# Kernel optimization log

Measured on AMD Instinct MI355X. Metric: run time of the kernel, lower is better.

## Reference

```python
import jax, jax.numpy as jnp
import numpy as np

MAX_EMBED = 1024
MAX_HEADS = 16
MIN_WIDTH_RATIO = 0.25


def setup_inputs() -> dict:
    key = jax.random.key(0)
    ks = jax.random.split(key, 10)
    B, S, E = 4, 1024, MAX_EMBED
    query = jax.random.normal(ks[0], (B, S, E), dtype=jnp.float32)
    attention_mask = jax.random.randint(ks[1], (B, 1, 1, S), 0, 2, dtype=jnp.int32)
    # SlimmableLinear params (max sizes); kaiming-ish scale ~ 1/sqrt(fan_in)
    scale = 1.0 / np.sqrt(E)
    def lin(kw, kb):
        w = jax.random.uniform(kw, (E, E), dtype=jnp.float32, minval=-scale, maxval=scale)
        b = jax.random.uniform(kb, (E,), dtype=jnp.float32, minval=-scale, maxval=scale)
        return w, b
    q_w, q_b = lin(ks[2], ks[3])
    k_w, k_b = lin(ks[4], ks[5])
    v_w, v_b = lin(ks[6], ks[7])
    o_w, o_b = lin(ks[8], ks[9])
    return {"query": query, "attention_mask": attention_mask,
            "q_w": q_w, "q_b": q_b, "k_w": k_w, "k_b": k_b,
            "v_w": v_w, "v_b": v_b, "o_w": o_w, "o_b": o_b,
            "width": 768}


def _slim_linear(x, w, b, width):
    # weight stored [out, in] like torch; slice to [width, width]
    return x[..., :width] @ w[:width, :width].T + b[:width]


def reference(query, attention_mask, q_w, q_b, k_w, k_b, v_w, v_b, o_w, o_b, width):
    min_width = int(MAX_EMBED * MIN_WIDTH_RATIO)
    width = max(min_width, min(int(width), MAX_EMBED))
    num_heads = max(1, width * MAX_HEADS // MAX_EMBED)
    head_dim = width // num_heads
    B, S, _ = query.shape

    q = _slim_linear(query, q_w, q_b, width)  # [B,S,width]
    k = _slim_linear(query, k_w, k_b, width)  # key=query (self-attn)
    v = _slim_linear(query, v_w, v_b, width)

    q = q.reshape(B, S, num_heads, head_dim).transpose(0, 2, 1, 3)  # [B,H,S,D]
    k = k.reshape(B, S, num_heads, head_dim).transpose(0, 2, 1, 3)
    v = v.reshape(B, S, num_heads, head_dim).transpose(0, 2, 1, 3)

    scores = jnp.einsum('bhqd,bhkd->bhqk', q, k) / jnp.sqrt(jnp.float32(head_dim))
    scores = jnp.where(attention_mask == 0, jnp.float32(-1e9), scores)
    attn_weights = jax.nn.softmax(scores, axis=-1)  # [B,H,S,S]
    attn_output = jnp.einsum('bhqk,bhkd->bhqd', attn_weights, v)
    attn_output = attn_output.transpose(0, 2, 1, 3).reshape(B, S, width)
    output = attn_output @ o_w[:width, :width].T + o_b[:width]
    return output, attn_weights
```

## Files before the change

kernel.cpp:

```cpp
#include <hip/hip_runtime.h>

#define Bn 4
#define Sn 1024
#define En 1024
#define Wn 768
#define Hn 12
#define Dn 64
#define XE ((size_t)Bn * Sn * Wn)

typedef __attribute__((ext_vector_type(8))) short short8;
typedef __attribute__((ext_vector_type(4))) short short4v;
typedef __attribute__((ext_vector_type(4))) float floatx4;

#define MFMA16(A, B, C) __builtin_amdgcn_mfma_f32_16x16x32_bf16(A, B, C, 0, 0, 0)

__device__ __forceinline__ unsigned short f2bf_rn(float f) {
    unsigned int u = __float_as_uint(f);
    unsigned int r = u + 0x7fffu + ((u >> 16) & 1u);
    return (unsigned short)(r >> 16);
}
__device__ __forceinline__ float bf2f(unsigned short h) {
    return __uint_as_float(((unsigned int)h) << 16);
}

__device__ __forceinline__ void gload_lds16(const unsigned short* g, unsigned short* l) {
    __builtin_amdgcn_global_load_lds(
        (const __attribute__((address_space(1))) void*)g,
        (__attribute__((address_space(3))) void*)l, 16, 0, 0);
}

__global__ __launch_bounds__(256) void prep_kernel(
    const float* __restrict__ x,
    const float* __restrict__ qw, const float* __restrict__ kw,
    const float* __restrict__ vw, const float* __restrict__ ow,
    const float* __restrict__ qb, const float* __restrict__ kb,
    const float* __restrict__ vb,
    unsigned short* __restrict__ xh, unsigned short* __restrict__ xl,
    unsigned short* __restrict__ wqh, unsigned short* __restrict__ wql,
    unsigned short* __restrict__ woh, unsigned short* __restrict__ wol,
    float* __restrict__ bq)
{
    const int bx = blockIdx.x;
    const float* src; unsigned short *dh, *dl; int e;
    if (bx < 3072) {
        e = (bx * 256 + threadIdx.x) * 4;
        src = x; dh = xh; dl = xl;
    } else if (bx < 3072 + 1728) {
        int bb = bx - 3072; int which = bb / 576;
        e = ((bb - which * 576) * 256 + threadIdx.x) * 4;
        src = (which == 0) ? qw : (which == 1) ? kw : vw;
        dh = wqh + (size_t)which * Wn * Wn;
        dl = wql + (size_t)which * Wn * Wn;
    } else if (bx < 3072 + 1728 + 576) {
        e = ((bx - 3072 - 1728) * 256 + threadIdx.x) * 4;
        src = ow; dh = woh; dl = wol;
    } else {
        int t = (bx - 3072 - 1728 - 576) * 256 + threadIdx.x;
        if (t < Wn) bq[t] = qb[t];
        else if (t < 2 * Wn) bq[t] = kb[t - Wn];
        else if (t < 3 * Wn) bq[t] = vb[t - 2 * Wn];
        return;
    }
    int row = e / Wn, col = e - row * Wn;
    float4 v = *(const float4*)(src + (size_t)row * En + col);
    float f[4] = {v.x, v.y, v.z, v.w};
    short4v h, l;
    #pragma unroll
    for (int i = 0; i < 4; ++i) {
        unsigned short hh = f2bf_rn(f[i]);
        h[i] = (short)hh;
        l[i] = (short)f2bf_rn(f[i] - bf2f(hh));
    }
    *(short4v*)(dh + e) = h;
    *(short4v*)(dl + e) = l;
}

__global__ __launch_bounds__(256) void qkv_mfma_kernel(
    const unsigned short* __restrict__ xh, const unsigned short* __restrict__ xl,
    const unsigned short* __restrict__ wh, const unsigned short* __restrict__ wl,
    const float* __restrict__ bq,
    unsigned short* __restrict__ qh_o, unsigned short* __restrict__ kh_o,
    unsigned short* __restrict__ vt_o)
{
    __shared__ __align__(16) unsigned short Ah[128 * 32];
    __shared__ __align__(16) unsigned short Al[128 * 32];
    __shared__ __align__(16) unsigned short Bh[128 * 32];
    __shared__ __align__(16) unsigned short Bl[128 * 32];

    const int tid = threadIdx.x;
    const int wave = tid >> 6, lane = tid & 63;
    const int quad = lane >> 4, l16 = lane & 15;
    const int m0 = blockIdx.x * 128, n0 = blockIdx.y * 128;
    const int wm = wave >> 1, wn = wave & 1;
    const int which = n0 / Wn;
    const bool full = (which == 2);

    floatx4 acc[4][4] = {};

    const unsigned short* gsrc = (wave == 0) ? xh : (wave == 1) ? xl
                               : (wave == 2) ? wh : wl;
    unsigned short* ldst = (wave == 0) ? Ah : (wave == 1) ? Al
                         : (wave == 2) ? Bh : Bl;
    const int base_row = (wave < 2) ? m0 : n0;
    const int r_in = lane >> 2;
    const int cs = (lane & 3) ^ (r_in & 3);

    for (int k0 = 0; k0 < Wn; k0 += 32) {
        if (full || wave != 1) {
            #pragma unroll
            for (int i = 0; i < 8; ++i) {
                int r = i * 16 + r_in;
                const unsigned short* gp =
                    gsrc + (size_t)(base_row + r) * Wn + k0 + cs * 8;
                gload_lds16(gp, ldst + i * 512);
            }
        }
        __syncthreads();

        short8 afh[4], afl[4], bfh[4], bfl[4];
        #pragma unroll
        for (int t = 0; t < 4; ++t) {
            int mr = wm * 64 + t * 16 + l16;
            int ca = quad ^ (mr & 3);
            afh[t] = *(const short8*)(Ah + mr * 32 + ca * 8);
            if (full) afl[t] = *(const short8*)(Al + mr * 32 + ca * 8);
            int nr = wn * 64 + t * 16 + l16;
            int cb = quad ^ (nr & 3);
            bfh[t] = *(const short8*)(Bh + nr * 32 + cb * 8);
            bfl[t] = *(const short8*)(Bl + nr * 32 + cb * 8);
        }
        #pragma unroll
        for (int mt = 0; mt < 4; ++mt)
            #pragma unroll
            for (int nt = 0; nt < 4; ++nt) {
                acc[mt][nt] = MFMA16(afh[mt], bfh[nt], acc[mt][nt]);
                acc[mt][nt] = MFMA16(afh[mt], bfl[nt], acc[mt][nt]);
                if (full) acc[mt][nt] = MFMA16(afl[mt], bfh[nt], acc[mt][nt]);
            }
        __syncthreads();
    }

    const int b = m0 >> 10;
    #pragma unroll
    for (int nt = 0; nt < 4; ++nt) {
        const int ng = n0 + wn * 64 + nt * 16 + l16;
        const float bias = bq[ng];
        const int f = ng - which * Wn;
        const int h = f >> 6, d = f & 63;
        #pragma unroll
        for (int mt = 0; mt < 4; ++mt) {
            const int mbase = m0 + wm * 64 + mt * 16 + quad * 4;
            const int s0 = mbase & (Sn - 1);
            if (which < 2) {
                unsigned short* oq = which ? kh_o : qh_o;
                size_t idx = (((size_t)(b * Hn + h)) * Sn + s0) * Dn + d;
                #pragma unroll
                for (int r = 0; r < 4; ++r)
                    oq[idx + (size_t)r * Dn] = f2bf_rn(acc[mt][nt][r] + bias);
            } else {
                size_t idx = (((size_t)(b * Hn + h)) * Dn + d) * Sn + s0;
                short4v pk;
                #pragma unroll
                for (int r = 0; r < 4; ++r)
                    pk[r] = (short)f2bf_rn(acc[mt][nt][r] + bias);
                *(short4v*)(vt_o + idx) = pk;
            }
        }
    }
}

__global__ __launch_bounds__(256) void attn_sum_kernel(
    const unsigned short* __restrict__ qh, const unsigned short* __restrict__ kh,
    const int* __restrict__ mask, float* __restrict__ lpart)
{
    const int tid = threadIdx.x;
    const int wave = tid >> 6, lane = tid & 63;
    const int quad = lane >> 4, l16 = lane & 15;
    const int qt = blockIdx.x >> 2, ks = blockIdx.x & 3;
    const int h = blockIdx.y, b = blockIdx.z;
    const int bh = b * Hn + h;
    const size_t kvb = (size_t)bh * Sn * Dn;

    short8 qf[2];
    {
        const int s = qt * 64 + wave * 16 + l16;
        const unsigned short* qp = qh + kvb + (size_t)s * Dn + quad * 8;
        qf[0] = *(const short8*)(qp);
        qf[1] = *(const short8*)(qp + 32);
    }

    float lsum[4] = {0.f, 0.f, 0.f, 0.f};

    for (int kt = 0; kt < 4; ++kt) {
        #pragma unroll
        for (int ct = 0; ct < 4; ++ct) {
            const int key = ks * 256 + kt * 64 + ct * 16 + l16;
            const unsigned short* kp = kh + kvb + (size_t)key * Dn + quad * 8;
            short8 kf0 = *(const short8*)(kp);
            short8 kf1 = *(const short8*)(kp + 32);
            floatx4 acc = {0.f, 0.f, 0.f, 0.f};
            acc = MFMA16(qf[0], kf0, acc);
            acc = MFMA16(qf[1], kf1, acc);
            const float mv = (float)mask[b * Sn + key];
            #pragma unroll
            for (int r = 0; r < 4; ++r)
                lsum[r] += __expf(acc[r] * 0.125f) * mv;
        }
    }

    #pragma unroll
    for (int r = 0; r < 4; ++r) {
        float v = lsum[r];
        v += __shfl_xor(v, 1, 64);
        v += __shfl_xor(v, 2, 64);
        v += __shfl_xor(v, 4, 64);
        v += __shfl_xor(v, 8, 64);
        lsum[r] = v;
    }
    if (l16 == 0) {
        const int row = qt * 64 + wave * 16 + quad * 4;
        #pragma unroll
        for (int r = 0; r < 4; ++r)
            lpart[((size_t)ks * Bn * Hn + bh) * Sn + row + r] = lsum[r];
    }
}

__global__ __launch_bounds__(256) void attn_out_kernel(
    const unsigned short* __restrict__ qh, const unsigned short* __restrict__ kh,
    const unsigned short* __restrict__ vt, const int* __restrict__ mask,
    const float* __restrict__ lpart, float* __restrict__ attn,
    unsigned short* __restrict__ aoh, unsigned short* __restrict__ aol)
{
    __shared__ __align__(16) unsigned short Ps[4][16 * 72];

    const int tid = threadIdx.x;
    const int wave = tid >> 6, lane = tid & 63;
    const int quad = lane >> 4, l16 = lane & 15;
    const int qt = blockIdx.x;
    const int h = blockIdx.y, b = blockIdx.z;
    const int bh = b * Hn + h;
    const size_t kvb = (size_t)bh * Sn * Dn;
    const size_t vbase = (size_t)bh * Dn * Sn;

    short8 qf[2];
    {
        const int s = qt * 64 + wave * 16 + l16;
        const unsigned short* qp = qh + kvb + (size_t)s * Dn + quad * 8;
        qf[0] = *(const short8*)(qp);
        qf[1] = *(const short8*)(qp + 32);
    }

    const int row0 = qt * 64 + wave * 16 + quad * 4;
    float li[4];
    #pragma unroll
    for (int r = 0; r < 4; ++r) {
        float lv = 0.f;
        #pragma unroll
        for (int s4 = 0; s4 < 4; ++s4)
            lv += lpart[((size_t)s4 * Bn * Hn + bh) * Sn + row0 + r];
        li[r] = (lv > 0.f) ? 1.f / lv : 0.f;
    }

    floatx4 oacc[4] = {};

    for (int kk = 0; kk < 16; ++kk) {
        const int k0 = kk * 64;
        #pragma unroll
        for (int ct = 0; ct < 4; ++ct) {
            const int key = k0 + ct * 16 + l16;
            const unsigned short* kp = kh + kvb + (size_t)key * Dn + quad * 8;
            short8 kf0 = *(const short8*)(kp);
            short8 kf1 = *(const short8*)(kp + 32);
            floatx4 acc = {0.f, 0.f, 0.f, 0.f};
            acc = MFMA16(qf[0], kf0, acc);
            acc = MFMA16(qf[1], kf1, acc);
            const float mv = (float)mask[b * Sn + key];
            #pragma unroll
            for (int r = 0; r < 4; ++r) {
                const float p = __expf(acc[r] * 0.125f) * mv * li[r];
                attn[((size_t)bh * Sn + row0 + r) * Sn + key] = p;
                Ps[wave][(quad * 4 + r) * 72 + ct * 16 + l16] = f2bf_rn(p);
            }
        }
        #pragma unroll
        for (int ksp = 0; ksp < 2; ++ksp) {
            short8 pf = *(const short8*)&Ps[wave][l16 * 72 + ksp * 32 + quad * 8];
            #pragma unroll
            for (int dt = 0; dt < 4; ++dt) {
                short8 vf = *(const short8*)(vt + vbase
                              + (size_t)(dt * 16 + l16) * Sn + k0 + ksp * 32 + quad * 8);
                oacc[dt] = MFMA16(pf, vf, oacc[dt]);
            }
        }
    }

    #pragma unroll
    for (int dt = 0; dt < 4; ++dt) {
        #pragma unroll
        for (int r = 0; r < 4; ++r) {
            const float o = oacc[dt][r];
            const unsigned short hh = f2bf_rn(o);
            const size_t idx = ((size_t)b * Sn + row0 + r) * Wn + h * Dn + dt * 16 + l16;
            aoh[idx] = hh;
            aol[idx] = f2bf_rn(o - bf2f(hh));
        }
    }
}

__global__ __launch_bounds__(256) void oproj_mfma_kernel(
    const unsigned short* __restrict__ aoh, const unsigned short* __restrict__ aol,
    const unsigned short* __restrict__ wh, const unsigned short* __restrict__ wl,
    const float* __restrict__ ob, float* __restrict__ out)
{
    __shared__ __align__(16) unsigned short Ah[64 * 32];
    __shared__ __align__(16) unsigned short Al[64 * 32];
    __shared__ __align__(16) unsigned short Bh[128 * 32];
    __shared__ __align__(16) unsigned short Bl[128 * 32];

    const int tid = threadIdx.x;
    const int wave = tid >> 6, lane = tid & 63;
    const int quad = lane >> 4, l16 = lane & 15;
    const int m0 = blockIdx.x * 64, n0 = blockIdx.y * 128;
    const int wm = wave >> 1, wn = wave & 1;

    floatx4 acc[2][4] = {};

    const int r_in = lane >> 2;
    const int cs = (lane & 3) ^ (r_in & 3);

    for (int k0 = 0; k0 < Wn; k0 += 32) {
        if (wave == 0) {
            #pragma unroll
            for (int i = 0; i < 4; ++i) {
                gload_lds16(aoh + (size_t)(m0 + i * 16 + r_in) * Wn + k0 + cs * 8,
                            Ah + i * 512);
                gload_lds16(aol + (size_t)(m0 + i * 16 + r_in) * Wn + k0 + cs * 8,
                            Al + i * 512);
            }
        } else if (wave == 1) {
            #pragma unroll
            for (int i = 0; i < 8; ++i)
                gload_lds16(wh + (size_t)(n0 + i * 16 + r_in) * Wn + k0 + cs * 8,
                            Bh + i * 512);
        } else if (wave == 2) {
            #pragma unroll
            for (int i = 0; i < 8; ++i)
                gload_lds16(wl + (size_t)(n0 + i * 16 + r_in) * Wn + k0 + cs * 8,
                            Bl + i * 512);
        }
        __syncthreads();

        short8 afh[2], afl[2], bfh[4], bfl[4];
        #pragma unroll
        for (int t = 0; t < 2; ++t) {
            int mr = wm * 32 + t * 16 + l16;
            int ca = quad ^ (mr & 3);
            afh[t] = *(const short8*)(Ah + mr * 32 + ca * 8);
            afl[t] = *(const short8*)(Al + mr * 32 + ca * 8);
        }
        #pragma unroll
        for (int t = 0; t < 4; ++t) {
            int nr = wn * 64 + t * 16 + l16;
            int cb = quad ^ (nr & 3);
            bfh[t] = *(const short8*)(Bh + nr * 32 + cb * 8);
            bfl[t] = *(const short8*)(Bl + nr * 32 + cb * 8);
        }
        #pragma unroll
        for (int mt = 0; mt < 2; ++mt)
            #pragma unroll
            for (int nt = 0; nt < 4; ++nt) {
                acc[mt][nt] = MFMA16(afh[mt], bfh[nt], acc[mt][nt]);
                acc[mt][nt] = MFMA16(afh[mt], bfl[nt], acc[mt][nt]);
                acc[mt][nt] = MFMA16(afl[mt], bfh[nt], acc[mt][nt]);
            }
        __syncthreads();
    }

    #pragma unroll
    for (int nt = 0; nt < 4; ++nt) {
        const int ng = n0 + wn * 64 + nt * 16 + l16;
        const float bias = ob[ng];
        #pragma unroll
        for (int mt = 0; mt < 2; ++mt) {
            const int m = m0 + wm * 32 + mt * 16 + quad * 4;
            #pragma unroll
            for (int r = 0; r < 4; ++r)
                out[(size_t)(m + r) * Wn + ng] = acc[mt][nt][r] + bias;
        }
    }
}

extern "C" void kernel_launch(void* const* d_in, const int* in_sizes, int n_in,
                              void* d_out, int out_size, void* d_ws, size_t ws_size,
                              hipStream_t stream) {
    const float* x    = (const float*)d_in[0];
    const int*   mask = (const int*)  d_in[1];
    const float* qw = (const float*)d_in[2];
    const float* qb = (const float*)d_in[3];
    const float* kw = (const float*)d_in[4];
    const float* kb = (const float*)d_in[5];
    const float* vw = (const float*)d_in[6];
    const float* vb = (const float*)d_in[7];
    const float* ow = (const float*)d_in[8];
    const float* ob = (const float*)d_in[9];

    float* out  = (float*)d_out;
    float* attn = out + XE;

    char* w = (char*)d_ws;
    unsigned short* xh   = (unsigned short*)w;  w += XE * 2;
    unsigned short* xl   = (unsigned short*)w;  w += XE * 2;
    unsigned short* wqh  = (unsigned short*)w;  w += (size_t)3 * Wn * Wn * 2;
    unsigned short* wql  = (unsigned short*)w;  w += (size_t)3 * Wn * Wn * 2;
    unsigned short* woh  = (unsigned short*)w;  w += (size_t)Wn * Wn * 2;
    unsigned short* wol  = (unsigned short*)w;  w += (size_t)Wn * Wn * 2;
    float*          bq   = (float*)w;           w += (size_t)3 * Wn * 4;
    unsigned short* qh   = (unsigned short*)w;  w += XE * 2;
    unsigned short* kh   = (unsigned short*)w;  w += XE * 2;
    unsigned short* vt_w = (unsigned short*)w;  w += XE * 2;
    float*          lpart = (float*)w;          w += (size_t)4 * Bn * Hn * Sn * 4;

    prep_kernel<<<5385, 256, 0, stream>>>(x, qw, kw, vw, ow, qb, kb, vb,
                                          xh, xl, wqh, wql, woh, wol, bq);

    qkv_mfma_kernel<<<dim3(32, 18), 256, 0, stream>>>(
        xh, xl, wqh, wql, bq, qh, kh, vt_w);

    attn_sum_kernel<<<dim3(64, Hn, Bn), 256, 0, stream>>>(
        qh, kh, mask, lpart);

    attn_out_kernel<<<dim3(16, Hn, Bn), 256, 0, stream>>>(
        qh, kh, vt_w, mask, lpart, attn, xh, xl);

    oproj_mfma_kernel<<<dim3(64, 6), 256, 0, stream>>>(
        xh, xl, woh, wol, ob, out);
}
```

Baseline: 462.5 us.

## Drop low-part MFMAs for Q/K, stage mask in LDS, vectorize attn writes from bf16

The QKV projection now runs only the hi*hi MFMA for the Q and K outputs and skips loading the low-part weight tiles, keeping the three-term split only for V. Both attention kernels stage the mask into shared memory as floats instead of re-reading the int mask per key. The attention-weights output is now written as row-contiguous float4 stores taken from the bf16-rounded P tile in LDS, replacing scattered per-element fp32 stores. These changes cut MFMA work, global load traffic and uncoalesced writes, but they lower the precision of Q/K and of the returned attention weights to bf16.

```diff
diff --git a/kernel.cpp b/kernel.cpp
--- a/kernel.cpp
+++ b/kernel.cpp
@@ -106,7 +106,7 @@
     const int cs = (lane & 3) ^ (r_in & 3);
 
     for (int k0 = 0; k0 < Wn; k0 += 32) {
-        if (full || wave != 1) {
+        if (full || wave == 0 || wave == 2) {
             #pragma unroll
             for (int i = 0; i < 8; ++i) {
                 int r = i * 16 + r_in;
@@ -127,15 +127,17 @@
             int nr = wn * 64 + t * 16 + l16;
             int cb = quad ^ (nr & 3);
             bfh[t] = *(const short8*)(Bh + nr * 32 + cb * 8);
-            bfl[t] = *(const short8*)(Bl + nr * 32 + cb * 8);
+            if (full) bfl[t] = *(const short8*)(Bl + nr * 32 + cb * 8);
         }
         #pragma unroll
         for (int mt = 0; mt < 4; ++mt)
             #pragma unroll
             for (int nt = 0; nt < 4; ++nt) {
                 acc[mt][nt] = MFMA16(afh[mt], bfh[nt], acc[mt][nt]);
-                acc[mt][nt] = MFMA16(afh[mt], bfl[nt], acc[mt][nt]);
-                if (full) acc[mt][nt] = MFMA16(afl[mt], bfh[nt], acc[mt][nt]);
+                if (full) {
+                    acc[mt][nt] = MFMA16(afh[mt], bfl[nt], acc[mt][nt]);
+                    acc[mt][nt] = MFMA16(afl[mt], bfh[nt], acc[mt][nt]);
+                }
             }
         __syncthreads();
     }
@@ -173,6 +175,8 @@
     const unsigned short* __restrict__ qh, const unsigned short* __restrict__ kh,
     const int* __restrict__ mask, float* __restrict__ lpart)
 {
+    __shared__ float msk[256];
+
     const int tid = threadIdx.x;
     const int wave = tid >> 6, lane = tid & 63;
     const int quad = lane >> 4, l16 = lane & 15;
@@ -181,6 +185,14 @@
     const int bh = b * Hn + h;
     const size_t kvb = (size_t)bh * Sn * Dn;
 
+    if (tid < 64) {
+        int4 mi = *(const int4*)(mask + b * Sn + ks * 256 + tid * 4);
+        msk[tid * 4 + 0] = (float)mi.x;
+        msk[tid * 4 + 1] = (float)mi.y;
+        msk[tid * 4 + 2] = (float)mi.z;
+        msk[tid * 4 + 3] = (float)mi.w;
+    }
+
     short8 qf[2];
     {
         const int s = qt * 64 + wave * 16 + l16;
@@ -188,20 +200,21 @@
         qf[0] = *(const short8*)(qp);
         qf[1] = *(const short8*)(qp + 32);
     }
+    __syncthreads();
 
     float lsum[4] = {0.f, 0.f, 0.f, 0.f};
 
     for (int kt = 0; kt < 4; ++kt) {
         #pragma unroll
         for (int ct = 0; ct < 4; ++ct) {
-            const int key = ks * 256 + kt * 64 + ct * 16 + l16;
-            const unsigned short* kp = kh + kvb + (size_t)key * Dn + quad * 8;
+            const int kl = kt * 64 + ct * 16 + l16;
+            const unsigned short* kp = kh + kvb + (size_t)(ks * 256 + kl) * Dn + quad * 8;
             short8 kf0 = *(const short8*)(kp);
             short8 kf1 = *(const short8*)(kp + 32);
             floatx4 acc = {0.f, 0.f, 0.f, 0.f};
             acc = MFMA16(qf[0], kf0, acc);
             acc = MFMA16(qf[1], kf1, acc);
-            const float mv = (float)mask[b * Sn + key];
+            const float mv = msk[kl];
             #pragma unroll
             for (int r = 0; r < 4; ++r)
                 lsum[r] += __expf(acc[r] * 0.125f) * mv;
@@ -232,6 +245,7 @@
     unsigned short* __restrict__ aoh, unsigned short* __restrict__ aol)
 {
     __shared__ __align__(16) unsigned short Ps[4][16 * 72];
+    __shared__ float msk[Sn];
 
     const int tid = threadIdx.x;
     const int wave = tid >> 6, lane = tid & 63;
@@ -242,6 +256,14 @@
     const size_t kvb = (size_t)bh * Sn * Dn;
     const size_t vbase = (size_t)bh * Dn * Sn;
 
+    {
+        int4 mi = *(const int4*)(mask + b * Sn + tid * 4);
+        msk[tid * 4 + 0] = (float)mi.x;
+        msk[tid * 4 + 1] = (float)mi.y;
+        msk[tid * 4 + 2] = (float)mi.z;
+        msk[tid * 4 + 3] = (float)mi.w;
+    }
+
     short8 qf[2];
     {
         const int s = qt * 64 + wave * 16 + l16;
@@ -260,8 +282,10 @@
             lv += lpart[((size_t)s4 * Bn * Hn + bh) * Sn + row0 + r];
         li[r] = (lv > 0.f) ? 1.f / lv : 0.f;
     }
+    __syncthreads();
 
     floatx4 oacc[4] = {};
+    float* aprow = attn + ((size_t)bh * Sn + qt * 64 + wave * 16 + l16) * Sn;
 
     for (int kk = 0; kk < 16; ++kk) {
         const int k0 = kk * 64;
@@ -274,17 +298,24 @@
             floatx4 acc = {0.f, 0.f, 0.f, 0.f};
             acc = MFMA16(qf[0], kf0, acc);
             acc = MFMA16(qf[1], kf1, acc);
-            const float mv = (float)mask[b * Sn + key];
+            const float mv = msk[key];
             #pragma unroll
             for (int r = 0; r < 4; ++r) {
                 const float p = __expf(acc[r] * 0.125f) * mv * li[r];
-                attn[((size_t)bh * Sn + row0 + r) * Sn + key] = p;
                 Ps[wave][(quad * 4 + r) * 72 + ct * 16 + l16] = f2bf_rn(p);
             }
         }
         #pragma unroll
         for (int ksp = 0; ksp < 2; ++ksp) {
             short8 pf = *(const short8*)&Ps[wave][l16 * 72 + ksp * 32 + quad * 8];
+            float4 f0, f1;
+            f0.x = bf2f((unsigned short)pf[0]); f0.y = bf2f((unsigned short)pf[1]);
+            f0.z = bf2f((unsigned short)pf[2]); f0.w = bf2f((unsigned short)pf[3]);
+            f1.x = bf2f((unsigned short)pf[4]); f1.y = bf2f((unsigned short)pf[5]);
+            f1.z = bf2f((unsigned short)pf[6]); f1.w = bf2f((unsigned short)pf[7]);
+            float* ap = aprow + k0 + ksp * 32 + quad * 8;
+            *(float4*)(ap)     = f0;
+            *(float4*)(ap + 4) = f1;
             #pragma unroll
             for (int dt = 0; dt < 4; ++dt) {
                 short8 vf = *(const short8*)(vt + vbase
```

Result: faster. 444.9 us (-3.8%).
